# Kernel optimization log

Measured on AMD Instinct MI355X. Metric: run time of the kernel, lower is better.

## Reference

```python
import jax, jax.numpy as jnp
import numpy as np
import math

N_PTS = 262144
STEP_LENGTH = math.sqrt(3.0) / 1024.0  # step_length = sqrt(3)/steps


def pos_enc(x):
    # classic NeRF frequency encoding: identity + sin/cos at 10 octaves -> 3 + 3*2*10 = 63
    freqs = 2.0 ** jnp.arange(10, dtype=x.dtype)            # [10]
    xb = x[..., :, None] * freqs                            # [N,3,10]
    xb = xb.reshape(x.shape[0], -1)                         # [N,30]
    return jnp.concatenate([x, jnp.sin(xb), jnp.cos(xb)], axis=-1)  # [N,63]


def dir_enc(u):
    # 26-dim frequency encoding of (dir+1)/2 (color head input 283 = 256 + 26 + 1).
    # 13 sin/cos pairs: per-channel octaves 2^0..2^4, truncated to 13 frequencies.
    freqs = 2.0 ** jnp.arange(5, dtype=u.dtype)             # [5]
    z = (u[..., :, None] * freqs).reshape(u.shape[0], -1)[:, :13]  # [N,13]
    return jnp.concatenate([jnp.sin(z), jnp.cos(z)], axis=-1)      # [N,26]


def linear(x, w, b):
    return x @ w.T + b


def setup_inputs() -> dict:
    key = jax.random.key(0)
    ks = jax.random.split(key, 16)
    s = 0.05
    inp = {
        "position": jax.random.uniform(ks[0], (N_PTS, 3), dtype=jnp.float32),
        "direction": jax.random.uniform(ks[1], (N_PTS, 3), dtype=jnp.float32, minval=-1.0, maxval=1.0),
        "w1_in": jax.random.normal(ks[2], (256, 63), jnp.float32) * s,
        "b1_in": jnp.zeros((256,), jnp.float32),
        "w1_h": jax.random.normal(ks[3], (3, 256, 256), jnp.float32) * s,
        "b1_h": jnp.zeros((3, 256), jnp.float32),
        "w2_in": jax.random.normal(ks[4], (256, 319), jnp.float32) * s,
        "b2_in": jnp.zeros((256,), jnp.float32),
        "w2_h": jax.random.normal(ks[5], (3, 256, 256), jnp.float32) * s,
        "b2_h": jnp.zeros((3, 256), jnp.float32),
        # sigma head Linear(256,1)
        "w_sigma": jax.random.normal(ks[6], (1, 256), jnp.float32) * s,
        "b_sigma": jnp.zeros((1,), jnp.float32),
        # color head Linear(283,128) -> ReLU -> Linear(128,3)
        "w_c1": jax.random.normal(ks[7], (128, 283), jnp.float32) * s,
        "b_c1": jnp.zeros((128,), jnp.float32),
        "w_c2": jax.random.normal(ks[8], (3, 128), jnp.float32) * s,
        "b_c2": jnp.zeros((3,), jnp.float32),
    }
    return inp


def reference(position, direction,
              w1_in, b1_in, w1_h, b1_h,
              w2_in, b2_in, w2_h, b2_h,
              w_sigma, b_sigma, w_c1, b_c1, w_c2, b_c2):
    pe = pos_enc(position)                                  # [N,63]
    h = jax.nn.relu(linear(pe, w1_in, b1_in))               # [N,256]
    for i in range(3):
        h = jax.nn.relu(linear(h, w1_h[i], b1_h[i]))
    g = jax.nn.relu(linear(jnp.concatenate([h, pe], axis=-1), w2_in, b2_in))  # [N,256]
    for i in range(3):
        g = jax.nn.relu(linear(g, w2_h[i], b2_h[i]))
    sigma_raw = linear(g, w_sigma, b_sigma)                 # [N,1]
    # get_alpha: 1 - exp(-relu(sigma) * step_length)
    alphas = 1.0 - jnp.exp(-jax.nn.relu(sigma_raw) * STEP_LENGTH)             # [N,1]
    # get_rgb: shares base features; concat [256 | 26 | 1] = 283
    de = dir_enc((direction + 1.0) * 0.5)                   # [N,26]
    feats = jnp.concatenate([g, de, sigma_raw], axis=-1)    # [N,283]
    rgb = jax.nn.sigmoid(linear(jax.nn.relu(linear(feats, w_c1, b_c1)), w_c2, b_c2))  # [N,3]
    return (rgb, alphas)
```

## Files before the change

kernel.cpp:

```cpp
#include <hip/hip_runtime.h>
#include <hip/hip_bf16.h>

#define N_PTS 262144
#define STEP_LEN 0.0016914558667664818f

using f32x4 = __attribute__((ext_vector_type(4))) float;
using s8 = __attribute__((ext_vector_type(8))) short;

__device__ __forceinline__ float bf2f(short s) {
    union { unsigned int u; float f; } v;
    v.u = ((unsigned int)(unsigned short)s) << 16;
    return v.f;
}
__device__ __forceinline__ short f2bf(float f) {
    __hip_bfloat16 h = __float2bfloat16(f);
    return *reinterpret_cast<short*>(&h);
}

#define OFF_W1    0
#define OFF_L1H0  16384
#define OFF_W2    212992
#define OFF_L2H0  294912
#define OFF_C1G   491520
#define OFF_C1DE  524288
#define OFF_WSIG  528384
#define OFF_WC2   528640
#define WS_ELEMS  532480

__device__ __forceinline__ float hid_val(const float* __restrict__ W, int e) {
    int j = e & 7, lane = (e >> 3) & 63, nt = (e >> 9) & 15, ks = e >> 13;
    int n = nt * 16 + (lane & 15), hi = lane >> 4;
    int f = ks * 32 + ((j >> 2) << 4) + hi * 4 + (j & 3);
    return W[n * 256 + f];
}

__global__ void prep_weights(const float* __restrict__ w1_in,
                             const float* __restrict__ w1_h,
                             const float* __restrict__ w2_in,
                             const float* __restrict__ w2_h,
                             const float* __restrict__ w_c1,
                             const float* __restrict__ w_sigma,
                             const float* __restrict__ w_c2,
                             __hip_bfloat16* __restrict__ ws) {
    int i = blockIdx.x * blockDim.x + threadIdx.x;
    if (i >= WS_ELEMS) return;
    float v;
    if (i < OFF_L1H0) {
        int e = i;
        int j = e & 7, lane = (e >> 3) & 63, nt = (e >> 9) & 15, ks = e >> 13;
        int n = nt * 16 + (lane & 15), hi = lane >> 4;
        int f = ks * 32 + hi * 8 + j;
        v = (f < 63) ? w1_in[n * 63 + f] : 0.f;
    } else if (i < OFF_W2) {
        int e = i - OFF_L1H0; int sub = e >> 16; e &= 65535;
        v = hid_val(w1_h + sub * 65536, e);
    } else if (i < OFF_L2H0) {
        int e = i - OFF_W2;
        int j = e & 7, lane = (e >> 3) & 63, nt = (e >> 9) & 15, ks = e >> 13;
        int n = nt * 16 + (lane & 15), hi = lane >> 4;
        if (ks < 8) {
            int f = ks * 32 + ((j >> 2) << 4) + hi * 4 + (j & 3);
            v = w2_in[n * 319 + f];
        } else {
            int pf = (ks - 8) * 32 + hi * 8 + j;
            v = (pf < 63) ? w2_in[n * 319 + 256 + pf] : 0.f;
        }
    } else if (i < OFF_C1G) {
        int e = i - OFF_L2H0; int sub = e >> 16; e &= 65535;
        v = hid_val(w2_h + sub * 65536, e);
    } else if (i < OFF_C1DE) {
        int e = i - OFF_C1G;
        int j = e & 7, lane = (e >> 3) & 63, nt = (e >> 9) & 7, ks = e >> 12;
        int n = nt * 16 + (lane & 15), hi = lane >> 4;
        int f = ks * 32 + ((j >> 2) << 4) + hi * 4 + (j & 3);
        v = w_c1[n * 283 + f];
    } else if (i < OFF_WSIG) {
        int e = i - OFF_C1DE;
        int j = e & 7, lane = (e >> 3) & 63, nt = (e >> 9) & 7;
        int n = nt * 16 + (lane & 15), hi = lane >> 4;
        int k = 256 + hi * 8 + j;
        v = (k < 283) ? w_c1[n * 283 + k] : 0.f;
    } else if (i < OFF_WC2) {
        int e = i - OFF_WSIG;
        int j = e & 7, hi = (e >> 3) & 3, ks = e >> 5;
        int f = ks * 32 + ((j >> 2) << 4) + hi * 4 + (j & 3);
        v = w_sigma[f];
    } else if (i < 529024) {
        int e = i - OFF_WC2;
        int j = e & 7, hi = (e >> 3) & 3, ks = (e >> 5) & 3, ch = e >> 7;
        int f = ks * 32 + ((j >> 2) << 4) + hi * 4 + (j & 3);
        v = w_c2[ch * 128 + f];
    } else {
        v = 0.f;
    }
    ws[i] = __float2bfloat16(v);
}

__device__ __forceinline__ float enc3(int f, float x0, float x1, float x2) {
    if (f < 3) return (f == 0) ? x0 : ((f == 1) ? x1 : x2);
    if (f < 33) {
        int q = f - 3; int c = q / 10, o = q % 10;
        float xc = (c == 0) ? x0 : ((c == 1) ? x1 : x2);
        return __sinf(xc * (float)(1 << o));
    }
    if (f < 63) {
        int q = f - 33; int c = q / 10, o = q % 10;
        float xc = (c == 0) ? x0 : ((c == 1) ? x1 : x2);
        return __cosf(xc * (float)(1 << o));
    }
    return 0.f;
}

#define MFMA16 __builtin_amdgcn_mfma_f32_16x16x32_bf16

#define STAGE4(BYTEOFF, DBUF) do { \
    const char* _src = wsB + (long)(BYTEOFF) + wid * 4096 + lane * 16; \
    char* _dst = (DBUF) + wid * 4096; \
    __builtin_amdgcn_global_load_lds((const unsigned int*)(_src),        (unsigned int*)(_dst),        16, 0, 0); \
    __builtin_amdgcn_global_load_lds((const unsigned int*)(_src + 1024), (unsigned int*)(_dst + 1024), 16, 0, 0); \
    __builtin_amdgcn_global_load_lds((const unsigned int*)(_src + 2048), (unsigned int*)(_dst + 2048), 16, 0, 0); \
    __builtin_amdgcn_global_load_lds((const unsigned int*)(_src + 3072), (unsigned int*)(_dst + 3072), 16, 0, 0); \
} while (0)

#define WKSTEP(RDBUF, STGOFF, WRBUF, A0, A1, FIRSTV) do { \
    STAGE4(STGOFF, WRBUF); \
    __builtin_amdgcn_s_setprio(1); \
    _Pragma("unroll") \
    for (int nt = 0; nt < 16; ++nt) { \
        const s8 w = *(const s8*)((RDBUF) + nt * 1024 + lane * 16); \
        acc[nt][0] = MFMA16(w, (A0), (FIRSTV) ? Z : acc[nt][0], 0, 0, 0); \
        acc[nt][1] = MFMA16(w, (A1), (FIRSTV) ? Z : acc[nt][1], 0, 0, 0); \
    } \
    __builtin_amdgcn_s_setprio(0); \
} while (0)

#define KBAR4 do { asm volatile("s_waitcnt vmcnt(4)" ::: "memory"); \
                   __builtin_amdgcn_s_barrier(); } while (0)
#define KBAR0 do { asm volatile("s_waitcnt vmcnt(0)" ::: "memory"); \
                   __builtin_amdgcn_s_barrier(); } while (0)

#define CONVERTL(BOFF) do { \
    _Pragma("unroll") \
    for (int nt = 0; nt < 16; ++nt) { \
        const f32x4 b4 = *(const f32x4*)(biasL + (((BOFF) + nt * 16 + hi4) << 2)); \
        _Pragma("unroll") \
        for (int r = 0; r < 4; ++r) { \
            actA[nt >> 1][((nt & 1) << 2) | r] = f2bf(fmaxf(acc[nt][0][r] + b4[r], 0.f)); \
            actB[nt >> 1][((nt & 1) << 2) | r] = f2bf(fmaxf(acc[nt][1][r] + b4[r], 0.f)); \
        } } } while (0)

#define CKSTEP(RDBUF, KS, FIRSTV) do { \
    __builtin_amdgcn_s_setprio(1); \
    _Pragma("unroll") \
    for (int nt = 0; nt < 8; ++nt) { \
        const s8 w = *(const s8*)((RDBUF) + nt * 1024 + lane * 16); \
        acc[nt][0] = MFMA16(w, actA[KS], (FIRSTV) ? Z : acc[nt][0], 0, 0, 0); \
        acc[nt][1] = MFMA16(w, actB[KS], (FIRSTV) ? Z : acc[nt][1], 0, 0, 0); \
    } \
    _Pragma("unroll") \
    for (int nt = 0; nt < 8; ++nt) { \
        const s8 w = *(const s8*)((RDBUF) + 8192 + nt * 1024 + lane * 16); \
        acc[nt][0] = MFMA16(w, actA[(KS) + 1], acc[nt][0], 0, 0, 0); \
        acc[nt][1] = MFMA16(w, actB[(KS) + 1], acc[nt][1], 0, 0, 0); \
    } \
    __builtin_amdgcn_s_setprio(0); \
} while (0)

__global__ __launch_bounds__(256, 2) void nerf_fused(
    const float* __restrict__ pos, const float* __restrict__ dir,
    const __hip_bfloat16* __restrict__ ws,
    const float* __restrict__ b1_in, const float* __restrict__ b1_h,
    const float* __restrict__ b2_in, const float* __restrict__ b2_h,
    const float* __restrict__ b_sigma, const float* __restrict__ b_c1,
    const float* __restrict__ b_c2,
    float* __restrict__ out) {

    __shared__ __align__(16) char Lds[74240];
    char* const S0 = Lds;
    char* const S1 = Lds + 16384;
    char* const S2 = Lds + 32768;
    char* const S3 = Lds + 49152;
    char* const biasL = Lds + 65536;

    const int t = threadIdx.x;
    const int lane = t & 63;
    const int wid = t >> 6;
    const int hi = lane >> 4;
    const int col = lane & 15;
    const int hi4 = hi * 4;
    const int row0 = blockIdx.x * 128;
    const int gA = row0 + wid * 32 + col;
    const int gB = gA + 16;
    const char* wsB = (const char*)ws;

    for (int i = t; i < 2176; i += 256) {
        float v;
        if (i < 256) v = b1_in[i];
        else if (i < 1024) v = b1_h[i - 256];
        else if (i < 1280) v = b2_in[i - 1024];
        else if (i < 2048) v = b2_h[i - 1280];
        else v = b_c1[i - 2048];
        *(float*)(biasL + i * 4) = v;
    }

    s8 peA0, peA1, peB0, peB1;
    {
        float xa0 = pos[gA*3], xa1 = pos[gA*3+1], xa2 = pos[gA*3+2];
        float xb0 = pos[gB*3], xb1 = pos[gB*3+1], xb2 = pos[gB*3+2];
#pragma unroll
        for (int j = 0; j < 8; ++j) {
            int f0 = hi * 8 + j, f1 = 32 + hi * 8 + j;
            peA0[j] = f2bf(enc3(f0, xa0, xa1, xa2));
            peA1[j] = f2bf(enc3(f1, xa0, xa1, xa2));
            peB0[j] = f2bf(enc3(f0, xb0, xb1, xb2));
            peB1[j] = f2bf(enc3(f1, xb0, xb1, xb2));
        }
    }

    f32x4 acc[16][2];
    s8 actA[8], actB[8];
    const f32x4 Z = {0.f, 0.f, 0.f, 0.f};

    STAGE4(0L, S0);
    STAGE4(16384L, S1);
    asm volatile("s_waitcnt vmcnt(4) lgkmcnt(0)" ::: "memory");
    __builtin_amdgcn_s_barrier();

    WKSTEP(S0, 2L*16384, S2, peA0, peB0, 1); KBAR4;
    WKSTEP(S1, 3L*16384, S3, peA1, peB1, 0); CONVERTL(0); KBAR4;

#pragma unroll 1
    for (int l = 0; l < 3; ++l) {
        const long lb = 65536L + (long)l * 131072;
        const int bo = 256 + (l << 8);
        WKSTEP(S2, lb,            S0, actA[0], actB[0], 1); KBAR4;
        WKSTEP(S3, lb + 16384,    S1, actA[1], actB[1], 0); KBAR4;
        WKSTEP(S0, lb + 2*16384,  S2, actA[2], actB[2], 0); KBAR4;
        WKSTEP(S1, lb + 3*16384,  S3, actA[3], actB[3], 0); KBAR4;
        WKSTEP(S2, lb + 4*16384,  S0, actA[4], actB[4], 0); KBAR4;
        WKSTEP(S3, lb + 5*16384,  S1, actA[5], actB[5], 0); KBAR4;
        WKSTEP(S0, lb + 6*16384,  S2, actA[6], actB[6], 0); KBAR4;
        WKSTEP(S1, lb + 7*16384,  S3, actA[7], actB[7], 0); CONVERTL(bo); KBAR4;
    }

    WKSTEP(S2, 28L*16384, S0, actA[0], actB[0], 1); KBAR4;
    WKSTEP(S3, 29L*16384, S1, actA[1], actB[1], 0); KBAR4;
    WKSTEP(S0, 30L*16384, S2, actA[2], actB[2], 0); KBAR4;
    WKSTEP(S1, 31L*16384, S3, actA[3], actB[3], 0); KBAR4;
    WKSTEP(S2, 32L*16384, S0, actA[4], actB[4], 0); KBAR4;
    WKSTEP(S3, 33L*16384, S1, actA[5], actB[5], 0); KBAR4;
    WKSTEP(S0, 34L*16384, S2, actA[6], actB[6], 0); KBAR4;
    WKSTEP(S1, 35L*16384, S3, actA[7], actB[7], 0); KBAR4;
    WKSTEP(S2, 36L*16384, S0, peA0,    peB0,    0); KBAR4;
    WKSTEP(S3, 37L*16384, S1, peA1,    peB1,    0); CONVERTL(1024); KBAR4;

#pragma unroll 1
    for (int l = 0; l < 3; ++l) {
        const long lb = (long)(38 + (l << 3)) * 16384;
        const int bo = 1280 + (l << 8);
        WKSTEP(S0, lb,            S2, actA[0], actB[0], 1); KBAR4;
        WKSTEP(S1, lb + 16384,    S3, actA[1], actB[1], 0); KBAR4;
        WKSTEP(S2, lb + 2*16384,  S0, actA[2], actB[2], 0); KBAR4;
        WKSTEP(S3, lb + 3*16384,  S1, actA[3], actB[3], 0); KBAR4;
        WKSTEP(S0, lb + 4*16384,  S2, actA[4], actB[4], 0); KBAR4;
        WKSTEP(S1, lb + 5*16384,  S3, actA[5], actB[5], 0); KBAR4;
        WKSTEP(S2, lb + 6*16384,  S0, actA[6], actB[6], 0); KBAR4;
        WKSTEP(S3, lb + 7*16384,  S1, actA[7], actB[7], 0); CONVERTL(bo); KBAR4;
    }

    float alphaA, alphaB, srA, srB;
    {
        float sA = 0.f, sB = 0.f;
#pragma unroll
        for (int ks = 0; ks < 8; ++ks) {
            const s8 wv = *(const s8*)(wsB + (OFF_WSIG + ks * 32 + hi * 8) * 2);
#pragma unroll
            for (int j = 0; j < 8; ++j) {
                sA += bf2f(actA[ks][j]) * bf2f(wv[j]);
                sB += bf2f(actB[ks][j]) * bf2f(wv[j]);
            }
        }
        sA += __shfl_xor(sA, 16); sA += __shfl_xor(sA, 32);
        sB += __shfl_xor(sB, 16); sB += __shfl_xor(sB, 32);
        srA = sA + b_sigma[0]; srB = sB + b_sigma[0];
        alphaA = 1.f - __expf(-fmaxf(srA, 0.f) * STEP_LEN);
        alphaB = 1.f - __expf(-fmaxf(srB, 0.f) * STEP_LEN);
    }

    s8 deA, deB;
    {
        float uA0 = (dir[gA*3+0] + 1.f) * 0.5f;
        float uA1 = (dir[gA*3+1] + 1.f) * 0.5f;
        float uA2 = (dir[gA*3+2] + 1.f) * 0.5f;
        float uB0 = (dir[gB*3+0] + 1.f) * 0.5f;
        float uB1 = (dir[gB*3+1] + 1.f) * 0.5f;
        float uB2 = (dir[gB*3+2] + 1.f) * 0.5f;
#pragma unroll
        for (int j = 0; j < 8; ++j) {
            int d = hi * 8 + j;
            float vA, vB;
            if (d < 13) {
                int c = d / 5, o = d % 5; float s = (float)(1 << o);
                vA = __sinf(((c == 0) ? uA0 : (c == 1) ? uA1 : uA2) * s);
                vB = __sinf(((c == 0) ? uB0 : (c == 1) ? uB1 : uB2) * s);
            } else if (d < 26) {
                int q = d - 13; int c = q / 5, o = q % 5; float s = (float)(1 << o);
                vA = __cosf(((c == 0) ? uA0 : (c == 1) ? uA1 : uA2) * s);
                vB = __cosf(((c == 0) ? uB0 : (c == 1) ? uB1 : uB2) * s);
            } else if (d == 26) {
                vA = srA; vB = srB;
            } else {
                vA = 0.f; vB = 0.f;
            }
            deA[j] = f2bf(vA); deB[j] = f2bf(vB);
        }
    }

    STAGE4(62L*16384, S2); CKSTEP(S0, 0, 1); KBAR4;
    STAGE4(63L*16384, S3); CKSTEP(S1, 2, 0); KBAR4;
    STAGE4(64L*16384, S0); CKSTEP(S2, 4, 0); KBAR4;
    CKSTEP(S3, 6, 0); KBAR0;
    {
        __builtin_amdgcn_s_setprio(1);
#pragma unroll
        for (int nt = 0; nt < 8; ++nt) {
            const s8 w = *(const s8*)(S0 + nt * 1024 + lane * 16);
            acc[nt][0] = MFMA16(w, deA, acc[nt][0], 0, 0, 0);
            acc[nt][1] = MFMA16(w, deB, acc[nt][1], 0, 0, 0);
        }
        __builtin_amdgcn_s_setprio(0);
    }

    s8 c1A[4], c1B[4];
#pragma unroll
    for (int nt = 0; nt < 8; ++nt) {
        const f32x4 b4 = *(const f32x4*)(biasL + ((2048 + nt * 16 + hi4) << 2));
#pragma unroll
        for (int r = 0; r < 4; ++r) {
            c1A[nt >> 1][((nt & 1) << 2) | r] = f2bf(fmaxf(acc[nt][0][r] + b4[r], 0.f));
            c1B[nt >> 1][((nt & 1) << 2) | r] = f2bf(fmaxf(acc[nt][1][r] + b4[r], 0.f));
        }
    }

#pragma unroll
    for (int ch = 0; ch < 3; ++ch) {
        float rA = 0.f, rB = 0.f;
#pragma unroll
        for (int ks = 0; ks < 4; ++ks) {
            const s8 wv = *(const s8*)(wsB + (OFF_WC2 + (ch * 4 + ks) * 32 + hi * 8) * 2);
#pragma unroll
            for (int j = 0; j < 8; ++j) {
                rA += bf2f(c1A[ks][j]) * bf2f(wv[j]);
                rB += bf2f(c1B[ks][j]) * bf2f(wv[j]);
            }
        }
        rA += __shfl_xor(rA, 16); rA += __shfl_xor(rA, 32);
        rB += __shfl_xor(rB, 16); rB += __shfl_xor(rB, 32);
        if (hi == 0) {
            out[gA * 3 + ch] = 1.f / (1.f + __expf(-(rA + b_c2[ch])));
            out[gB * 3 + ch] = 1.f / (1.f + __expf(-(rB + b_c2[ch])));
        }
    }
    if (hi == 0) {
        out[3 * N_PTS + gA] = alphaA;
        out[3 * N_PTS + gB] = alphaB;
    }
}

extern "C" void kernel_launch(void* const* d_in, const int* in_sizes, int n_in,
                              void* d_out, int out_size, void* d_ws, size_t ws_size,
                              hipStream_t stream) {
    const float* position = (const float*)d_in[0];
    const float* direction = (const float*)d_in[1];
    const float* w1_in = (const float*)d_in[2];
    const float* b1_in = (const float*)d_in[3];
    const float* w1_h  = (const float*)d_in[4];
    const float* b1_h  = (const float*)d_in[5];
    const float* w2_in = (const float*)d_in[6];
    const float* b2_in = (const float*)d_in[7];
    const float* w2_h  = (const float*)d_in[8];
    const float* b2_h  = (const float*)d_in[9];
    const float* w_sigma = (const float*)d_in[10];
    const float* b_sigma = (const float*)d_in[11];
    const float* w_c1  = (const float*)d_in[12];
    const float* b_c1  = (const float*)d_in[13];
    const float* w_c2  = (const float*)d_in[14];
    const float* b_c2  = (const float*)d_in[15];
    float* out = (float*)d_out;
    __hip_bfloat16* ws = (__hip_bfloat16*)d_ws;

    prep_weights<<<(WS_ELEMS + 255) / 256, 256, 0, stream>>>(
        w1_in, w1_h, w2_in, w2_h, w_c1, w_sigma, w_c2, ws);

    nerf_fused<<<N_PTS / 128, 256, 0, stream>>>(
        position, direction, ws,
        b1_in, b1_h, b2_in, b2_h,
        b_sigma, b_c1, b_c2, out);
}
```

Before: 240.3 us.

## Stage weights in 32KB double-buffered chunks, halving barriers per layer

Weight staging switches from a four-buffer ring of 16KB chunks with a vmcnt(4) wait to two 32KB buffers. Each step loads 8KB per wave and runs two k-steps of MFMAs between barriers. The first weight chunk is now issued before the bias copy and the positional encoding, so those loads overlap with that setup work. The sigma value is patched into the direction encoding after sigma is computed. This halves the number of barrier points, at the cost of a full vmcnt(0) wait at each barrier and less prefetch depth than the old two-ahead ring.

```diff
diff --git a/kernel.cpp b/kernel.cpp
--- a/kernel.cpp
+++ b/kernel.cpp
@@ -113,31 +113,36 @@
 
 #define MFMA16 __builtin_amdgcn_mfma_f32_16x16x32_bf16
 
-#define STAGE4(BYTEOFF, DBUF) do { \
-    const char* _src = wsB + (long)(BYTEOFF) + wid * 4096 + lane * 16; \
-    char* _dst = (DBUF) + wid * 4096; \
-    __builtin_amdgcn_global_load_lds((const unsigned int*)(_src),        (unsigned int*)(_dst),        16, 0, 0); \
-    __builtin_amdgcn_global_load_lds((const unsigned int*)(_src + 1024), (unsigned int*)(_dst + 1024), 16, 0, 0); \
-    __builtin_amdgcn_global_load_lds((const unsigned int*)(_src + 2048), (unsigned int*)(_dst + 2048), 16, 0, 0); \
-    __builtin_amdgcn_global_load_lds((const unsigned int*)(_src + 3072), (unsigned int*)(_dst + 3072), 16, 0, 0); \
+#define GLL(SRC, DST) __builtin_amdgcn_global_load_lds( \
+    (const unsigned int*)(SRC), (unsigned int*)(DST), 16, 0, 0)
+
+#define STAGE8(BYTEOFF, DBUF) do { \
+    const char* _src = wsB + (long)(BYTEOFF) + wid * 8192 + lane * 16; \
+    char* _dst = (DBUF) + wid * 8192; \
+    GLL(_src,        _dst);        GLL(_src + 1024, _dst + 1024); \
+    GLL(_src + 2048, _dst + 2048); GLL(_src + 3072, _dst + 3072); \
+    GLL(_src + 4096, _dst + 4096); GLL(_src + 5120, _dst + 5120); \
+    GLL(_src + 6144, _dst + 6144); GLL(_src + 7168, _dst + 7168); \
 } while (0)
 
-#define WKSTEP(RDBUF, STGOFF, WRBUF, A0, A1, FIRSTV) do { \
-    STAGE4(STGOFF, WRBUF); \
-    __builtin_amdgcn_s_setprio(1); \
+#define WHALF(RD, SUB, A0, A1, FIRSTV) do { \
     _Pragma("unroll") \
     for (int nt = 0; nt < 16; ++nt) { \
-        const s8 w = *(const s8*)((RDBUF) + nt * 1024 + lane * 16); \
+        const s8 w = *(const s8*)((RD) + (SUB) + nt * 1024 + lane * 16); \
         acc[nt][0] = MFMA16(w, (A0), (FIRSTV) ? Z : acc[nt][0], 0, 0, 0); \
         acc[nt][1] = MFMA16(w, (A1), (FIRSTV) ? Z : acc[nt][1], 0, 0, 0); \
-    } \
-    __builtin_amdgcn_s_setprio(0); \
-} while (0)
-
-#define KBAR4 do { asm volatile("s_waitcnt vmcnt(4)" ::: "memory"); \
-                   __builtin_amdgcn_s_barrier(); } while (0)
-#define KBAR0 do { asm volatile("s_waitcnt vmcnt(0)" ::: "memory"); \
-                   __builtin_amdgcn_s_barrier(); } while (0)
+    } } while (0)
+
+#define CHALF(RD, SUB, A0, A1, FIRSTV) do { \
+    _Pragma("unroll") \
+    for (int nt = 0; nt < 8; ++nt) { \
+        const s8 w = *(const s8*)((RD) + (SUB) + nt * 1024 + lane * 16); \
+        acc[nt][0] = MFMA16(w, (A0), (FIRSTV) ? Z : acc[nt][0], 0, 0, 0); \
+        acc[nt][1] = MFMA16(w, (A1), (FIRSTV) ? Z : acc[nt][1], 0, 0, 0); \
+    } } while (0)
+
+#define PBAR do { asm volatile("s_waitcnt vmcnt(0)" ::: "memory"); \
+                  __builtin_amdgcn_s_barrier(); } while (0)
 
 #define CONVERTL(BOFF) do { \
     _Pragma("unroll") \
@@ -149,21 +154,34 @@
             actB[nt >> 1][((nt & 1) << 2) | r] = f2bf(fmaxf(acc[nt][1][r] + b4[r], 0.f)); \
         } } } while (0)
 
-#define CKSTEP(RDBUF, KS, FIRSTV) do { \
-    __builtin_amdgcn_s_setprio(1); \
-    _Pragma("unroll") \
-    for (int nt = 0; nt < 8; ++nt) { \
-        const s8 w = *(const s8*)((RDBUF) + nt * 1024 + lane * 16); \
-        acc[nt][0] = MFMA16(w, actA[KS], (FIRSTV) ? Z : acc[nt][0], 0, 0, 0); \
-        acc[nt][1] = MFMA16(w, actB[KS], (FIRSTV) ? Z : acc[nt][1], 0, 0, 0); \
-    } \
-    _Pragma("unroll") \
-    for (int nt = 0; nt < 8; ++nt) { \
-        const s8 w = *(const s8*)((RDBUF) + 8192 + nt * 1024 + lane * 16); \
-        acc[nt][0] = MFMA16(w, actA[(KS) + 1], acc[nt][0], 0, 0, 0); \
-        acc[nt][1] = MFMA16(w, actB[(KS) + 1], acc[nt][1], 0, 0, 0); \
-    } \
-    __builtin_amdgcn_s_setprio(0); \
+#define LAYER4_ODD(CB, BO) do { \
+    STAGE8((CB) +  32768, B0); __builtin_amdgcn_s_setprio(1); \
+    WHALF(B1, 0, actA[0], actB[0], 1); WHALF(B1, 16384, actA[1], actB[1], 0); \
+    __builtin_amdgcn_s_setprio(0); PBAR; \
+    STAGE8((CB) +  65536, B1); __builtin_amdgcn_s_setprio(1); \
+    WHALF(B0, 0, actA[2], actB[2], 0); WHALF(B0, 16384, actA[3], actB[3], 0); \
+    __builtin_amdgcn_s_setprio(0); PBAR; \
+    STAGE8((CB) +  98304, B0); __builtin_amdgcn_s_setprio(1); \
+    WHALF(B1, 0, actA[4], actB[4], 0); WHALF(B1, 16384, actA[5], actB[5], 0); \
+    __builtin_amdgcn_s_setprio(0); PBAR; \
+    STAGE8((CB) + 131072, B1); __builtin_amdgcn_s_setprio(1); \
+    WHALF(B0, 0, actA[6], actB[6], 0); WHALF(B0, 16384, actA[7], actB[7], 0); \
+    __builtin_amdgcn_s_setprio(0); CONVERTL(BO); PBAR; \
+} while (0)
+
+#define LAYER4_EVEN(CB, BO) do { \
+    STAGE8((CB) +  32768, B1); __builtin_amdgcn_s_setprio(1); \
+    WHALF(B0, 0, actA[0], actB[0], 1); WHALF(B0, 16384, actA[1], actB[1], 0); \
+    __builtin_amdgcn_s_setprio(0); PBAR; \
+    STAGE8((CB) +  65536, B0); __builtin_amdgcn_s_setprio(1); \
+    WHALF(B1, 0, actA[2], actB[2], 0); WHALF(B1, 16384, actA[3], actB[3], 0); \
+    __builtin_amdgcn_s_setprio(0); PBAR; \
+    STAGE8((CB) +  98304, B1); __builtin_amdgcn_s_setprio(1); \
+    WHALF(B0, 0, actA[4], actB[4], 0); WHALF(B0, 16384, actA[5], actB[5], 0); \
+    __builtin_amdgcn_s_setprio(0); PBAR; \
+    STAGE8((CB) + 131072, B0); __builtin_amdgcn_s_setprio(1); \
+    WHALF(B1, 0, actA[6], actB[6], 0); WHALF(B1, 16384, actA[7], actB[7], 0); \
+    __builtin_amdgcn_s_setprio(0); CONVERTL(BO); PBAR; \
 } while (0)
 
 __global__ __launch_bounds__(256, 2) void nerf_fused(
@@ -176,10 +194,8 @@
     float* __restrict__ out) {
 
     __shared__ __align__(16) char Lds[74240];
-    char* const S0 = Lds;
-    char* const S1 = Lds + 16384;
-    char* const S2 = Lds + 32768;
-    char* const S3 = Lds + 49152;
+    char* const B0 = Lds;
+    char* const B1 = Lds + 32768;
     char* const biasL = Lds + 65536;
 
     const int t = threadIdx.x;
@@ -193,6 +209,8 @@
     const int gB = gA + 16;
     const char* wsB = (const char*)ws;
 
+    STAGE8(0L, B0);
+
     for (int i = t; i < 2176; i += 256) {
         float v;
         if (i < 256) v = b1_in[i];
@@ -217,76 +235,6 @@
         }
     }
 
-    f32x4 acc[16][2];
-    s8 actA[8], actB[8];
-    const f32x4 Z = {0.f, 0.f, 0.f, 0.f};
-
-    STAGE4(0L, S0);
-    STAGE4(16384L, S1);
-    asm volatile("s_waitcnt vmcnt(4) lgkmcnt(0)" ::: "memory");
-    __builtin_amdgcn_s_barrier();
-
-    WKSTEP(S0, 2L*16384, S2, peA0, peB0, 1); KBAR4;
-    WKSTEP(S1, 3L*16384, S3, peA1, peB1, 0); CONVERTL(0); KBAR4;
-
-#pragma unroll 1
-    for (int l = 0; l < 3; ++l) {
-        const long lb = 65536L + (long)l * 131072;
-        const int bo = 256 + (l << 8);
-        WKSTEP(S2, lb,            S0, actA[0], actB[0], 1); KBAR4;
-        WKSTEP(S3, lb + 16384,    S1, actA[1], actB[1], 0); KBAR4;
-        WKSTEP(S0, lb + 2*16384,  S2, actA[2], actB[2], 0); KBAR4;
-        WKSTEP(S1, lb + 3*16384,  S3, actA[3], actB[3], 0); KBAR4;
-        WKSTEP(S2, lb + 4*16384,  S0, actA[4], actB[4], 0); KBAR4;
-        WKSTEP(S3, lb + 5*16384,  S1, actA[5], actB[5], 0); KBAR4;
-        WKSTEP(S0, lb + 6*16384,  S2, actA[6], actB[6], 0); KBAR4;
-        WKSTEP(S1, lb + 7*16384,  S3, actA[7], actB[7], 0); CONVERTL(bo); KBAR4;
-    }
-
-    WKSTEP(S2, 28L*16384, S0, actA[0], actB[0], 1); KBAR4;
-    WKSTEP(S3, 29L*16384, S1, actA[1], actB[1], 0); KBAR4;
-    WKSTEP(S0, 30L*16384, S2, actA[2], actB[2], 0); KBAR4;
-    WKSTEP(S1, 31L*16384, S3, actA[3], actB[3], 0); KBAR4;
-    WKSTEP(S2, 32L*16384, S0, actA[4], actB[4], 0); KBAR4;
-    WKSTEP(S3, 33L*16384, S1, actA[5], actB[5], 0); KBAR4;
-    WKSTEP(S0, 34L*16384, S2, actA[6], actB[6], 0); KBAR4;
-    WKSTEP(S1, 35L*16384, S3, actA[7], actB[7], 0); KBAR4;
-    WKSTEP(S2, 36L*16384, S0, peA0,    peB0,    0); KBAR4;
-    WKSTEP(S3, 37L*16384, S1, peA1,    peB1,    0); CONVERTL(1024); KBAR4;
-
-#pragma unroll 1
-    for (int l = 0; l < 3; ++l) {
-        const long lb = (long)(38 + (l << 3)) * 16384;
-        const int bo = 1280 + (l << 8);
-        WKSTEP(S0, lb,            S2, actA[0], actB[0], 1); KBAR4;
-        WKSTEP(S1, lb + 16384,    S3, actA[1], actB[1], 0); KBAR4;
-        WKSTEP(S2, lb + 2*16384,  S0, actA[2], actB[2], 0); KBAR4;
-        WKSTEP(S3, lb + 3*16384,  S1, actA[3], actB[3], 0); KBAR4;
-        WKSTEP(S0, lb + 4*16384,  S2, actA[4], actB[4], 0); KBAR4;
-        WKSTEP(S1, lb + 5*16384,  S3, actA[5], actB[5], 0); KBAR4;
-        WKSTEP(S2, lb + 6*16384,  S0, actA[6], actB[6], 0); KBAR4;
-        WKSTEP(S3, lb + 7*16384,  S1, actA[7], actB[7], 0); CONVERTL(bo); KBAR4;
-    }
-
-    float alphaA, alphaB, srA, srB;
-    {
-        float sA = 0.f, sB = 0.f;
-#pragma unroll
-        for (int ks = 0; ks < 8; ++ks) {
-            const s8 wv = *(const s8*)(wsB + (OFF_WSIG + ks * 32 + hi * 8) * 2);
-#pragma unroll
-            for (int j = 0; j < 8; ++j) {
-                sA += bf2f(actA[ks][j]) * bf2f(wv[j]);
-                sB += bf2f(actB[ks][j]) * bf2f(wv[j]);
-            }
-        }
-        sA += __shfl_xor(sA, 16); sA += __shfl_xor(sA, 32);
-        sB += __shfl_xor(sB, 16); sB += __shfl_xor(sB, 32);
-        srA = sA + b_sigma[0]; srB = sB + b_sigma[0];
-        alphaA = 1.f - __expf(-fmaxf(srA, 0.f) * STEP_LEN);
-        alphaB = 1.f - __expf(-fmaxf(srB, 0.f) * STEP_LEN);
-    }
-
     s8 deA, deB;
     {
         float uA0 = (dir[gA*3+0] + 1.f) * 0.5f;
@@ -298,7 +246,7 @@
 #pragma unroll
         for (int j = 0; j < 8; ++j) {
             int d = hi * 8 + j;
-            float vA, vB;
+            float vA = 0.f, vB = 0.f;
             if (d < 13) {
                 int c = d / 5, o = d % 5; float s = (float)(1 << o);
                 vA = __sinf(((c == 0) ? uA0 : (c == 1) ? uA1 : uA2) * s);
@@ -307,29 +255,102 @@
                 int q = d - 13; int c = q / 5, o = q % 5; float s = (float)(1 << o);
                 vA = __cosf(((c == 0) ? uA0 : (c == 1) ? uA1 : uA2) * s);
                 vB = __cosf(((c == 0) ? uB0 : (c == 1) ? uB1 : uB2) * s);
-            } else if (d == 26) {
-                vA = srA; vB = srB;
-            } else {
-                vA = 0.f; vB = 0.f;
             }
             deA[j] = f2bf(vA); deB[j] = f2bf(vB);
         }
     }
 
-    STAGE4(62L*16384, S2); CKSTEP(S0, 0, 1); KBAR4;
-    STAGE4(63L*16384, S3); CKSTEP(S1, 2, 0); KBAR4;
-    STAGE4(64L*16384, S0); CKSTEP(S2, 4, 0); KBAR4;
-    CKSTEP(S3, 6, 0); KBAR0;
+    f32x4 acc[16][2];
+    s8 actA[8], actB[8];
+    const f32x4 Z = {0.f, 0.f, 0.f, 0.f};
+
+    asm volatile("s_waitcnt vmcnt(0) lgkmcnt(0)" ::: "memory");
+    __builtin_amdgcn_s_barrier();
+
+    STAGE8(1L*32768, B1);
+    __builtin_amdgcn_s_setprio(1);
+    WHALF(B0, 0, peA0, peB0, 1); WHALF(B0, 16384, peA1, peB1, 0);
+    __builtin_amdgcn_s_setprio(0);
+    CONVERTL(0); PBAR;
+
+#pragma unroll 1
+    for (int l = 0; l < 3; ++l)
+        LAYER4_ODD(32768L + (long)l * 131072, 256 + (l << 8));
+
+    STAGE8(14L*32768, B0);
+    __builtin_amdgcn_s_setprio(1);
+    WHALF(B1, 0, actA[0], actB[0], 1); WHALF(B1, 16384, actA[1], actB[1], 0);
+    __builtin_amdgcn_s_setprio(0); PBAR;
+    STAGE8(15L*32768, B1);
+    __builtin_amdgcn_s_setprio(1);
+    WHALF(B0, 0, actA[2], actB[2], 0); WHALF(B0, 16384, actA[3], actB[3], 0);
+    __builtin_amdgcn_s_setprio(0); PBAR;
+    STAGE8(16L*32768, B0);
+    __builtin_amdgcn_s_setprio(1);
+    WHALF(B1, 0, actA[4], actB[4], 0); WHALF(B1, 16384, actA[5], actB[5], 0);
+    __builtin_amdgcn_s_setprio(0); PBAR;
+    STAGE8(17L*32768, B1);
+    __builtin_amdgcn_s_setprio(1);
+    WHALF(B0, 0, actA[6], actB[6], 0); WHALF(B0, 16384, actA[7], actB[7], 0);
+    __builtin_amdgcn_s_setprio(0); PBAR;
+    STAGE8(18L*32768, B0);
+    __builtin_amdgcn_s_setprio(1);
+    WHALF(B1, 0, peA0, peB0, 0); WHALF(B1, 16384, peA1, peB1, 0);
+    __builtin_amdgcn_s_setprio(0);
+    CONVERTL(1024); PBAR;
+
+#pragma unroll 1
+    for (int l = 0; l < 3; ++l)
+        LAYER4_EVEN(589824L + (long)l * 131072, 1280 + (l << 8));
+
+    float srA, srB, alphaA, alphaB;
     {
-        __builtin_amdgcn_s_setprio(1);
-#pragma unroll
-        for (int nt = 0; nt < 8; ++nt) {
-            const s8 w = *(const s8*)(S0 + nt * 1024 + lane * 16);
-            acc[nt][0] = MFMA16(w, deA, acc[nt][0], 0, 0, 0);
-            acc[nt][1] = MFMA16(w, deB, acc[nt][1], 0, 0, 0);
-        }
-        __builtin_amdgcn_s_setprio(0);
-    }
+        float sA = 0.f, sB = 0.f;
+#pragma unroll
+        for (int ks = 0; ks < 8; ++ks) {
+            const s8 wv = *(const s8*)(wsB + (OFF_WSIG + ks * 32 + hi * 8) * 2);
+#pragma unroll
+            for (int j = 0; j < 8; ++j) {
+                sA += bf2f(actA[ks][j]) * bf2f(wv[j]);
+                sB += bf2f(actB[ks][j]) * bf2f(wv[j]);
+            }
+        }
+        sA += __shfl_xor(sA, 16); sA += __shfl_xor(sA, 32);
+        sB += __shfl_xor(sB, 16); sB += __shfl_xor(sB, 32);
+        srA = sA + b_sigma[0]; srB = sB + b_sigma[0];
+        alphaA = 1.f - __expf(-fmaxf(srA, 0.f) * STEP_LEN);
+        alphaB = 1.f - __expf(-fmaxf(srB, 0.f) * STEP_LEN);
+        if (hi == 3) { deA[2] = f2bf(srA); deB[2] = f2bf(srB); }
+    }
+
+    STAGE8(31L*32768, B1);
+    __builtin_amdgcn_s_setprio(1);
+    CHALF(B0, 0,     actA[0], actB[0], 1);
+    CHALF(B0, 8192,  actA[1], actB[1], 0);
+    CHALF(B0, 16384, actA[2], actB[2], 0);
+    CHALF(B0, 24576, actA[3], actB[3], 0);
+    __builtin_amdgcn_s_setprio(0); PBAR;
+
+    {
+        const char* _src = wsB + 1048576L + wid * 2048 + lane * 16;
+        char* _dst = B0 + wid * 2048;
+        GLL(_src, _dst); GLL(_src + 1024, _dst + 1024);
+    }
+    __builtin_amdgcn_s_setprio(1);
+    CHALF(B1, 0,     actA[4], actB[4], 0);
+    CHALF(B1, 8192,  actA[5], actB[5], 0);
+    CHALF(B1, 16384, actA[6], actB[6], 0);
+    CHALF(B1, 24576, actA[7], actB[7], 0);
+    __builtin_amdgcn_s_setprio(0); PBAR;
+
+    __builtin_amdgcn_s_setprio(1);
+#pragma unroll
+    for (int nt = 0; nt < 8; ++nt) {
+        const s8 w = *(const s8*)(B0 + nt * 1024 + lane * 16);
+        acc[nt][0] = MFMA16(w, deA, acc[nt][0], 0, 0, 0);
+        acc[nt][1] = MFMA16(w, deB, acc[nt][1], 0, 0, 0);
+    }
+    __builtin_amdgcn_s_setprio(0);
 
     s8 c1A[4], c1B[4];
 #pragma unroll
```

After: 243.3 us. Within noise of the previous version (+1.2%).

## Triple-buffer weight staging and store biases as bf16 to fit three blocks per CU

Applied to the files above, without the earlier changes.

Shrinks the weight staging ring in LDS from four 16KB buffers to three, rotated through pointer swaps, and stores biases in LDS as bf16 instead of fp32. Together these cut LDS from about 74KB to about 53KB, and launch bounds rise to 3 blocks per CU for higher occupancy. The first weight stage is issued before the bias fill, and direction encoding is hoisted ahead of the MLP, to overlap those loads with setup. Risks: a shallower prefetch ring with vmcnt(4) waits, register pressure under the tighter launch bound possibly causing spills, and small precision loss from bf16 biases.

```diff
diff --git a/kernel.cpp b/kernel.cpp
--- a/kernel.cpp
+++ b/kernel.cpp
@@ -6,6 +6,7 @@
 
 using f32x4 = __attribute__((ext_vector_type(4))) float;
 using s8 = __attribute__((ext_vector_type(8))) short;
+using s4 = __attribute__((ext_vector_type(4))) short;
 
 __device__ __forceinline__ float bf2f(short s) {
     union { unsigned int u; float f; } v;
@@ -113,25 +114,29 @@
 
 #define MFMA16 __builtin_amdgcn_mfma_f32_16x16x32_bf16
 
+#define GLL(SRC, DST) __builtin_amdgcn_global_load_lds( \
+    (const unsigned int*)(SRC), (unsigned int*)(DST), 16, 0, 0)
+
 #define STAGE4(BYTEOFF, DBUF) do { \
     const char* _src = wsB + (long)(BYTEOFF) + wid * 4096 + lane * 16; \
     char* _dst = (DBUF) + wid * 4096; \
-    __builtin_amdgcn_global_load_lds((const unsigned int*)(_src),        (unsigned int*)(_dst),        16, 0, 0); \
-    __builtin_amdgcn_global_load_lds((const unsigned int*)(_src + 1024), (unsigned int*)(_dst + 1024), 16, 0, 0); \
-    __builtin_amdgcn_global_load_lds((const unsigned int*)(_src + 2048), (unsigned int*)(_dst + 2048), 16, 0, 0); \
-    __builtin_amdgcn_global_load_lds((const unsigned int*)(_src + 3072), (unsigned int*)(_dst + 3072), 16, 0, 0); \
+    GLL(_src,        _dst);        GLL(_src + 1024, _dst + 1024); \
+    GLL(_src + 2048, _dst + 2048); GLL(_src + 3072, _dst + 3072); \
 } while (0)
+
+#define SP1 __builtin_amdgcn_s_setprio(1)
+#define SP0 __builtin_amdgcn_s_setprio(0)
 
 #define WKSTEP(RDBUF, STGOFF, WRBUF, A0, A1, FIRSTV) do { \
     STAGE4(STGOFF, WRBUF); \
-    __builtin_amdgcn_s_setprio(1); \
+    SP1; \
     _Pragma("unroll") \
     for (int nt = 0; nt < 16; ++nt) { \
         const s8 w = *(const s8*)((RDBUF) + nt * 1024 + lane * 16); \
         acc[nt][0] = MFMA16(w, (A0), (FIRSTV) ? Z : acc[nt][0], 0, 0, 0); \
         acc[nt][1] = MFMA16(w, (A1), (FIRSTV) ? Z : acc[nt][1], 0, 0, 0); \
     } \
-    __builtin_amdgcn_s_setprio(0); \
+    SP0; \
 } while (0)
 
 #define KBAR4 do { asm volatile("s_waitcnt vmcnt(4)" ::: "memory"); \
@@ -142,15 +147,16 @@
 #define CONVERTL(BOFF) do { \
     _Pragma("unroll") \
     for (int nt = 0; nt < 16; ++nt) { \
-        const f32x4 b4 = *(const f32x4*)(biasL + (((BOFF) + nt * 16 + hi4) << 2)); \
+        const s4 bv = *(const s4*)(biasL + (((BOFF) + nt * 16 + hi4) << 1)); \
         _Pragma("unroll") \
         for (int r = 0; r < 4; ++r) { \
-            actA[nt >> 1][((nt & 1) << 2) | r] = f2bf(fmaxf(acc[nt][0][r] + b4[r], 0.f)); \
-            actB[nt >> 1][((nt & 1) << 2) | r] = f2bf(fmaxf(acc[nt][1][r] + b4[r], 0.f)); \
+            float bb = bf2f(bv[r]); \
+            actA[nt >> 1][((nt & 1) << 2) | r] = f2bf(fmaxf(acc[nt][0][r] + bb, 0.f)); \
+            actB[nt >> 1][((nt & 1) << 2) | r] = f2bf(fmaxf(acc[nt][1][r] + bb, 0.f)); \
         } } } while (0)
 
 #define CKSTEP(RDBUF, KS, FIRSTV) do { \
-    __builtin_amdgcn_s_setprio(1); \
+    SP1; \
     _Pragma("unroll") \
     for (int nt = 0; nt < 8; ++nt) { \
         const s8 w = *(const s8*)((RDBUF) + nt * 1024 + lane * 16); \
@@ -163,10 +169,10 @@
         acc[nt][0] = MFMA16(w, actA[(KS) + 1], acc[nt][0], 0, 0, 0); \
         acc[nt][1] = MFMA16(w, actB[(KS) + 1], acc[nt][1], 0, 0, 0); \
     } \
-    __builtin_amdgcn_s_setprio(0); \
+    SP0; \
 } while (0)
 
-__global__ __launch_bounds__(256, 2) void nerf_fused(
+__global__ __launch_bounds__(256, 3) void nerf_fused(
     const float* __restrict__ pos, const float* __restrict__ dir,
     const __hip_bfloat16* __restrict__ ws,
     const float* __restrict__ b1_in, const float* __restrict__ b1_h,
@@ -175,23 +181,23 @@
     const float* __restrict__ b_c2,
     float* __restrict__ out) {
 
-    __shared__ __align__(16) char Lds[74240];
-    char* const S0 = Lds;
-    char* const S1 = Lds + 16384;
-    char* const S2 = Lds + 32768;
-    char* const S3 = Lds + 49152;
-    char* const biasL = Lds + 65536;
+    __shared__ __align__(16) char Lds[53504];
+    char* const B0 = Lds;
+    char* const B1 = Lds + 16384;
+    char* const B2 = Lds + 32768;
+    char* const biasL = Lds + 49152;
 
     const int t = threadIdx.x;
     const int lane = t & 63;
     const int wid = t >> 6;
     const int hi = lane >> 4;
-    const int col = lane & 15;
     const int hi4 = hi * 4;
     const int row0 = blockIdx.x * 128;
-    const int gA = row0 + wid * 32 + col;
+    const int gA = row0 + wid * 32 + (lane & 15);
     const int gB = gA + 16;
     const char* wsB = (const char*)ws;
+
+    STAGE4(0L, B0);
 
     for (int i = t; i < 2176; i += 256) {
         float v;
@@ -200,7 +206,7 @@
         else if (i < 1280) v = b2_in[i - 1024];
         else if (i < 2048) v = b2_h[i - 1280];
         else v = b_c1[i - 2048];
-        *(float*)(biasL + i * 4) = v;
+        *(short*)(biasL + i * 2) = f2bf(v);
     }
 
     s8 peA0, peA1, peB0, peB1;
@@ -215,76 +221,6 @@
             peB0[j] = f2bf(enc3(f0, xb0, xb1, xb2));
             peB1[j] = f2bf(enc3(f1, xb0, xb1, xb2));
         }
-    }
-
-    f32x4 acc[16][2];
-    s8 actA[8], actB[8];
-    const f32x4 Z = {0.f, 0.f, 0.f, 0.f};
-
-    STAGE4(0L, S0);
-    STAGE4(16384L, S1);
-    asm volatile("s_waitcnt vmcnt(4) lgkmcnt(0)" ::: "memory");
-    __builtin_amdgcn_s_barrier();
-
-    WKSTEP(S0, 2L*16384, S2, peA0, peB0, 1); KBAR4;
-    WKSTEP(S1, 3L*16384, S3, peA1, peB1, 0); CONVERTL(0); KBAR4;
-
-#pragma unroll 1
-    for (int l = 0; l < 3; ++l) {
-        const long lb = 65536L + (long)l * 131072;
-        const int bo = 256 + (l << 8);
-        WKSTEP(S2, lb,            S0, actA[0], actB[0], 1); KBAR4;
-        WKSTEP(S3, lb + 16384,    S1, actA[1], actB[1], 0); KBAR4;
-        WKSTEP(S0, lb + 2*16384,  S2, actA[2], actB[2], 0); KBAR4;
-        WKSTEP(S1, lb + 3*16384,  S3, actA[3], actB[3], 0); KBAR4;
-        WKSTEP(S2, lb + 4*16384,  S0, actA[4], actB[4], 0); KBAR4;
-        WKSTEP(S3, lb + 5*16384,  S1, actA[5], actB[5], 0); KBAR4;
-        WKSTEP(S0, lb + 6*16384,  S2, actA[6], actB[6], 0); KBAR4;
-        WKSTEP(S1, lb + 7*16384,  S3, actA[7], actB[7], 0); CONVERTL(bo); KBAR4;
-    }
-
-    WKSTEP(S2, 28L*16384, S0, actA[0], actB[0], 1); KBAR4;
-    WKSTEP(S3, 29L*16384, S1, actA[1], actB[1], 0); KBAR4;
-    WKSTEP(S0, 30L*16384, S2, actA[2], actB[2], 0); KBAR4;
-    WKSTEP(S1, 31L*16384, S3, actA[3], actB[3], 0); KBAR4;
-    WKSTEP(S2, 32L*16384, S0, actA[4], actB[4], 0); KBAR4;
-    WKSTEP(S3, 33L*16384, S1, actA[5], actB[5], 0); KBAR4;
-    WKSTEP(S0, 34L*16384, S2, actA[6], actB[6], 0); KBAR4;
-    WKSTEP(S1, 35L*16384, S3, actA[7], actB[7], 0); KBAR4;
-    WKSTEP(S2, 36L*16384, S0, peA0,    peB0,    0); KBAR4;
-    WKSTEP(S3, 37L*16384, S1, peA1,    peB1,    0); CONVERTL(1024); KBAR4;
-
-#pragma unroll 1
-    for (int l = 0; l < 3; ++l) {
-        const long lb = (long)(38 + (l << 3)) * 16384;
-        const int bo = 1280 + (l << 8);
-        WKSTEP(S0, lb,            S2, actA[0], actB[0], 1); KBAR4;
-        WKSTEP(S1, lb + 16384,    S3, actA[1], actB[1], 0); KBAR4;
-        WKSTEP(S2, lb + 2*16384,  S0, actA[2], actB[2], 0); KBAR4;
-        WKSTEP(S3, lb + 3*16384,  S1, actA[3], actB[3], 0); KBAR4;
-        WKSTEP(S0, lb + 4*16384,  S2, actA[4], actB[4], 0); KBAR4;
-        WKSTEP(S1, lb + 5*16384,  S3, actA[5], actB[5], 0); KBAR4;
-        WKSTEP(S2, lb + 6*16384,  S0, actA[6], actB[6], 0); KBAR4;
-        WKSTEP(S3, lb + 7*16384,  S1, actA[7], actB[7], 0); CONVERTL(bo); KBAR4;
-    }
-
-    float alphaA, alphaB, srA, srB;
-    {
-        float sA = 0.f, sB = 0.f;
-#pragma unroll
-        for (int ks = 0; ks < 8; ++ks) {
-            const s8 wv = *(const s8*)(wsB + (OFF_WSIG + ks * 32 + hi * 8) * 2);
-#pragma unroll
-            for (int j = 0; j < 8; ++j) {
-                sA += bf2f(actA[ks][j]) * bf2f(wv[j]);
-                sB += bf2f(actB[ks][j]) * bf2f(wv[j]);
-            }
-        }
-        sA += __shfl_xor(sA, 16); sA += __shfl_xor(sA, 32);
-        sB += __shfl_xor(sB, 16); sB += __shfl_xor(sB, 32);
-        srA = sA + b_sigma[0]; srB = sB + b_sigma[0];
-        alphaA = 1.f - __expf(-fmaxf(srA, 0.f) * STEP_LEN);
-        alphaB = 1.f - __expf(-fmaxf(srB, 0.f) * STEP_LEN);
     }
 
     s8 deA, deB;
@@ -298,7 +234,7 @@
 #pragma unroll
         for (int j = 0; j < 8; ++j) {
             int d = hi * 8 + j;
-            float vA, vB;
+            float vA = 0.f, vB = 0.f;
             if (d < 13) {
                 int c = d / 5, o = d % 5; float s = (float)(1 << o);
                 vA = __sinf(((c == 0) ? uA0 : (c == 1) ? uA1 : uA2) * s);
@@ -307,38 +243,111 @@
                 int q = d - 13; int c = q / 5, o = q % 5; float s = (float)(1 << o);
                 vA = __cosf(((c == 0) ? uA0 : (c == 1) ? uA1 : uA2) * s);
                 vB = __cosf(((c == 0) ? uB0 : (c == 1) ? uB1 : uB2) * s);
-            } else if (d == 26) {
-                vA = srA; vB = srB;
-            } else {
-                vA = 0.f; vB = 0.f;
             }
             deA[j] = f2bf(vA); deB[j] = f2bf(vB);
         }
     }
 
-    STAGE4(62L*16384, S2); CKSTEP(S0, 0, 1); KBAR4;
-    STAGE4(63L*16384, S3); CKSTEP(S1, 2, 0); KBAR4;
-    STAGE4(64L*16384, S0); CKSTEP(S2, 4, 0); KBAR4;
-    CKSTEP(S3, 6, 0); KBAR0;
+    f32x4 acc[16][2];
+    s8 actA[8], actB[8];
+    const f32x4 Z = {0.f, 0.f, 0.f, 0.f};
+
+    STAGE4(16384L, B1);
+    asm volatile("s_waitcnt vmcnt(4) lgkmcnt(0)" ::: "memory");
+    __builtin_amdgcn_s_barrier();
+
+    WKSTEP(B0, 2L*16384, B2, peA0, peB0, 1); KBAR4;
+    WKSTEP(B1, 3L*16384, B0, peA1, peB1, 0); CONVERTL(0); KBAR4;
+
     {
-        __builtin_amdgcn_s_setprio(1);
-#pragma unroll
-        for (int nt = 0; nt < 8; ++nt) {
-            const s8 w = *(const s8*)(S0 + nt * 1024 + lane * 16);
-            acc[nt][0] = MFMA16(w, deA, acc[nt][0], 0, 0, 0);
-            acc[nt][1] = MFMA16(w, deB, acc[nt][1], 0, 0, 0);
-        }
-        __builtin_amdgcn_s_setprio(0);
-    }
+        char* q0 = B2; char* q1 = B0; char* q2 = B1;
+#pragma unroll 1
+        for (int l = 0; l < 3; ++l) {
+            const long sb = 65536L + (long)l * 131072;
+            const int bo = 256 + (l << 8);
+            WKSTEP(q0, sb,           q2, actA[0], actB[0], 1); KBAR4;
+            WKSTEP(q1, sb + 16384,   q0, actA[1], actB[1], 0); KBAR4;
+            WKSTEP(q2, sb + 2*16384, q1, actA[2], actB[2], 0); KBAR4;
+            WKSTEP(q0, sb + 3*16384, q2, actA[3], actB[3], 0); KBAR4;
+            WKSTEP(q1, sb + 4*16384, q0, actA[4], actB[4], 0); KBAR4;
+            WKSTEP(q2, sb + 5*16384, q1, actA[5], actB[5], 0); KBAR4;
+            WKSTEP(q0, sb + 6*16384, q2, actA[6], actB[6], 0); KBAR4;
+            WKSTEP(q1, sb + 7*16384, q0, actA[7], actB[7], 0); CONVERTL(bo); KBAR4;
+            char* tq = q2; q2 = q1; q1 = q0; q0 = tq;
+        }
+    }
+
+    WKSTEP(B2, 28L*16384, B1, actA[0], actB[0], 1); KBAR4;
+    WKSTEP(B0, 29L*16384, B2, actA[1], actB[1], 0); KBAR4;
+    WKSTEP(B1, 30L*16384, B0, actA[2], actB[2], 0); KBAR4;
+    WKSTEP(B2, 31L*16384, B1, actA[3], actB[3], 0); KBAR4;
+    WKSTEP(B0, 32L*16384, B2, actA[4], actB[4], 0); KBAR4;
+    WKSTEP(B1, 33L*16384, B0, actA[5], actB[5], 0); KBAR4;
+    WKSTEP(B2, 34L*16384, B1, actA[6], actB[6], 0); KBAR4;
+    WKSTEP(B0, 35L*16384, B2, actA[7], actB[7], 0); KBAR4;
+    WKSTEP(B1, 36L*16384, B0, peA0,    peB0,    0); KBAR4;
+    WKSTEP(B2, 37L*16384, B1, peA1,    peB1,    0); CONVERTL(1024); KBAR4;
+
+    {
+        char* q0 = B0; char* q1 = B1; char* q2 = B2;
+#pragma unroll 1
+        for (int l = 0; l < 3; ++l) {
+            const long sb = (long)(38 + (l << 3)) * 16384;
+            const int bo = 1280 + (l << 8);
+            WKSTEP(q0, sb,           q2, actA[0], actB[0], 1); KBAR4;
+            WKSTEP(q1, sb + 16384,   q0, actA[1], actB[1], 0); KBAR4;
+            WKSTEP(q2, sb + 2*16384, q1, actA[2], actB[2], 0); KBAR4;
+            WKSTEP(q0, sb + 3*16384, q2, actA[3], actB[3], 0); KBAR4;
+            WKSTEP(q1, sb + 4*16384, q0, actA[4], actB[4], 0); KBAR4;
+            WKSTEP(q2, sb + 5*16384, q1, actA[5], actB[5], 0); KBAR4;
+            WKSTEP(q0, sb + 6*16384, q2, actA[6], actB[6], 0); KBAR4;
+            WKSTEP(q1, sb + 7*16384, q0, actA[7], actB[7], 0); CONVERTL(bo); KBAR4;
+            char* tq = q2; q2 = q1; q1 = q0; q0 = tq;
+        }
+    }
+
+    float srA, srB, alphaA, alphaB;
+    {
+        float sA = 0.f, sB = 0.f;
+#pragma unroll
+        for (int ks = 0; ks < 8; ++ks) {
+            const s8 wv = *(const s8*)(wsB + (OFF_WSIG + ks * 32 + hi * 8) * 2);
+#pragma unroll
+            for (int j = 0; j < 8; ++j) {
+                sA += bf2f(actA[ks][j]) * bf2f(wv[j]);
+                sB += bf2f(actB[ks][j]) * bf2f(wv[j]);
+            }
+        }
+        sA += __shfl_xor(sA, 16); sA += __shfl_xor(sA, 32);
+        sB += __shfl_xor(sB, 16); sB += __shfl_xor(sB, 32);
+        srA = sA + b_sigma[0]; srB = sB + b_sigma[0];
+        alphaA = 1.f - __expf(-fmaxf(srA, 0.f) * STEP_LEN);
+        alphaB = 1.f - __expf(-fmaxf(srB, 0.f) * STEP_LEN);
+        if (hi == 3) { deA[2] = f2bf(srA); deB[2] = f2bf(srB); }
+    }
+
+    STAGE4(62L*16384, B2); CKSTEP(B0, 0, 1); KBAR4;
+    STAGE4(63L*16384, B0); CKSTEP(B1, 2, 0); KBAR4;
+    STAGE4(64L*16384, B1); CKSTEP(B2, 4, 0); KBAR4;
+    CKSTEP(B0, 6, 0); KBAR0;
+    SP1;
+#pragma unroll
+    for (int nt = 0; nt < 8; ++nt) {
+        const s8 w = *(const s8*)(B1 + nt * 1024 + lane * 16);
+        acc[nt][0] = MFMA16(w, deA, acc[nt][0], 0, 0, 0);
+        acc[nt][1] = MFMA16(w, deB, acc[nt][1], 0, 0, 0);
+    }
+    SP0;
 
     s8 c1A[4], c1B[4];
 #pragma unroll
     for (int nt = 0; nt < 8; ++nt) {
-        const f32x4 b4 = *(const f32x4*)(biasL + ((2048 + nt * 16 + hi4) << 2));
+        const s4 bv = *(const s4*)(biasL + ((2048 + nt * 16 + hi4) << 1));
 #pragma unroll
         for (int r = 0; r < 4; ++r) {
-            c1A[nt >> 1][((nt & 1) << 2) | r] = f2bf(fmaxf(acc[nt][0][r] + b4[r], 0.f));
-            c1B[nt >> 1][((nt & 1) << 2) | r] = f2bf(fmaxf(acc[nt][1][r] + b4[r], 0.f));
+            float bb = bf2f(bv[r]);
+            c1A[nt >> 1][((nt & 1) << 2) | r] = f2bf(fmaxf(acc[nt][0][r] + bb, 0.f));
+            c1B[nt >> 1][((nt & 1) << 2) | r] = f2bf(fmaxf(acc[nt][1][r] + bb, 0.f));
         }
     }
 
```

After: 465.9 us. 1.94x slower.
